# Kernel optimization log

Hardware: AMD Instinct MI355X
Metric: run time of the kernel (lower is better)

## Reference

```python
import jax, jax.numpy as jnp
import numpy as np

N_NODES = 50000
NEG_SLOPE = 0.2  # PyG GATConv default leaky_relu slope


def gat_conv(x, W, att_src, att_dst, bias, src, dst, num_nodes, concat):
    """PyG-style GATConv (eval mode, self-loops already appended to src/dst)."""
    H, C = att_src.shape
    h = (x @ W).reshape(num_nodes, H, C)           # [N,H,C]
    a_s = jnp.einsum('nhc,hc->nh', h, att_src)     # [N,H]
    a_d = jnp.einsum('nhc,hc->nh', h, att_dst)     # [N,H]
    e = jax.nn.leaky_relu(a_s[src] + a_d[dst], NEG_SLOPE)   # [E,H]
    # segment softmax over incoming edges of each destination node
    m = jax.ops.segment_max(e, dst, num_segments=num_nodes)  # [N,H]
    p = jnp.exp(e - m[dst])
    denom = jax.ops.segment_sum(p, dst, num_segments=num_nodes)
    alpha = p / (denom[dst] + 1e-16)               # [E,H]
    # scatter-aggregate messages
    out = jax.ops.segment_sum(h[src] * alpha[:, :, None], dst,
                              num_segments=num_nodes)        # [N,H,C]
    out = out.reshape(num_nodes, H * C) if concat else out.mean(axis=1)
    return out + bias


def setup_inputs() -> dict:
    key = jax.random.key(0)
    ks = jax.random.split(key, 12)
    F_in, H1, C1, C2 = 500, 8, 64, 64
    E = 600000
    x = jax.random.normal(ks[0], (N_NODES, F_in), jnp.float32)
    edge_index = jax.random.randint(ks[1], (2, E), 0, N_NODES, jnp.int64)
    s = 0.1
    return {
        'x': x,
        'edge_index': edge_index,
        'W1': jax.random.normal(ks[2], (F_in, H1 * C1), jnp.float32) * s,
        'att_src1': jax.random.normal(ks[3], (H1, C1), jnp.float32) * s,
        'att_dst1': jax.random.normal(ks[4], (H1, C1), jnp.float32) * s,
        'b1': jax.random.normal(ks[5], (H1 * C1,), jnp.float32) * s,
        'W2': jax.random.normal(ks[6], (H1 * C1, C2), jnp.float32) * s,
        'att_src2': jax.random.normal(ks[7], (1, C2), jnp.float32) * s,
        'att_dst2': jax.random.normal(ks[8], (1, C2), jnp.float32) * s,
        'b2': jax.random.normal(ks[9], (C2,), jnp.float32) * s,
        'Wl': jax.random.normal(ks[10], (C2, F_in), jnp.float32) * s,
        'bl': jax.random.normal(ks[11], (F_in,), jnp.float32) * s,
    }


def reference(x, edge_index, W1, att_src1, att_dst1, b1,
              W2, att_src2, att_dst2, b2, Wl, bl):
    # eval mode: F.dropout(p=0.6) is identity
    loop = jnp.arange(N_NODES, dtype=edge_index.dtype)
    src = jnp.concatenate([edge_index[0], loop])  # add_self_loops=True default
    dst = jnp.concatenate([edge_index[1], loop])
    h = gat_conv(x, W1, att_src1, att_dst1, b1, src, dst, N_NODES, concat=True)
    h = jax.nn.elu(h)
    h = gat_conv(h, W2, att_src2, att_dst2, b2, src, dst, N_NODES, concat=False)
    h = jax.nn.elu(h)
    return h @ Wl + bl
```

## Files before the change

kernel.cpp:

```cpp
#include <hip/hip_runtime.h>
#include <hip/hip_bf16.h>


#define N_NODES 50000
#define F_IN    500
#define H1      8
#define E_RAW   600000
#define E_TOT   (E_RAW + N_NODES)
#define NEG_SLOPE 0.2f

#define MP      50048
#define KP      512

typedef __attribute__((ext_vector_type(8))) short bf16x8;
typedef __attribute__((ext_vector_type(4))) float f32x4;
typedef unsigned short ushort_t;

__device__ __forceinline__ int edge_src(const int* ei, int e) {
    return (e < E_RAW) ? ei[e] : e - E_RAW;
}
__device__ __forceinline__ int edge_dst(const int* ei, int e) {
    return (e < E_RAW) ? ei[E_RAW + e] : e - E_RAW;
}

__device__ __forceinline__ unsigned short f32_to_bf16(float f) {
    unsigned int u = __float_as_uint(f);
    u += 0x7fffu + ((u >> 16) & 1u);
    return (unsigned short)(u >> 16);
}
__device__ __forceinline__ float bf16_lo(unsigned int u) {
    return __uint_as_float(u << 16);
}
__device__ __forceinline__ float bf16_hi(unsigned int u) {
    return __uint_as_float(u & 0xffff0000u);
}

__global__ void fill_i32(int* __restrict__ p, int v, long n) {
    long i = blockIdx.x * (long)blockDim.x + threadIdx.x;
    long stride = (long)gridDim.x * blockDim.x;
    for (; i < n; i += stride) p[i] = v;
}

__global__ void count_deg(const int* __restrict__ ei, int* __restrict__ deg) {
    long i = blockIdx.x * (long)blockDim.x + threadIdx.x;
    long stride = (long)gridDim.x * blockDim.x;
    for (; i < E_TOT; i += stride) atomicAdd(&deg[edge_dst(ei, (int)i)], 1);
}

__global__ void scan_part(const int* __restrict__ deg, int* __restrict__ part, int n) {
    __shared__ int sm[256];
    int i = blockIdx.x * 256 + threadIdx.x;
    sm[threadIdx.x] = (i < n) ? deg[i] : 0;
    __syncthreads();
    for (int d = 128; d >= 1; d >>= 1) {
        if (threadIdx.x < d) sm[threadIdx.x] += sm[threadIdx.x + d];
        __syncthreads();
    }
    if (threadIdx.x == 0) part[blockIdx.x] = sm[0];
}

__global__ void scan_top(int* __restrict__ part, int nb) {
    __shared__ int sm[256];
    int t = threadIdx.x;
    sm[t] = (t < nb) ? part[t] : 0;
    __syncthreads();
    for (int d = 1; d < 256; d <<= 1) {
        int v = (t >= d) ? sm[t - d] : 0;
        __syncthreads();
        sm[t] += v;
        __syncthreads();
    }
    if (t < nb) part[t] = (t == 0) ? 0 : sm[t - 1];
}

__global__ void scan_final(const int* __restrict__ deg, const int* __restrict__ part,
                           int* __restrict__ off, int n) {
    __shared__ int sm[256];
    int i = blockIdx.x * 256 + threadIdx.x;
    int v = (i < n) ? deg[i] : 0;
    sm[threadIdx.x] = v;
    __syncthreads();
    for (int d = 1; d < 256; d <<= 1) {
        int u = (threadIdx.x >= d) ? sm[threadIdx.x - d] : 0;
        __syncthreads();
        sm[threadIdx.x] += u;
        __syncthreads();
    }
    int excl = sm[threadIdx.x] - v + part[blockIdx.x];
    if (i < n) off[i] = excl;
    if (i == n - 1) off[n] = excl + v;
}

__global__ void scatter_edges(const int* __restrict__ ei, const int* __restrict__ off,
                              int* __restrict__ cnt, int* __restrict__ eid) {
    long i = blockIdx.x * (long)blockDim.x + threadIdx.x;
    long stride = (long)gridDim.x * blockDim.x;
    for (; i < E_TOT; i += stride) {
        int d = edge_dst(ei, (int)i);
        int p = atomicAdd(&cnt[d], 1);
        eid[off[d] + p] = (int)i;
    }
}

__global__ void cvt_w1t_bf16(const float* __restrict__ W1, ushort_t* __restrict__ w1t) {
    int idx = blockIdx.x * blockDim.x + threadIdx.x;
    if (idx >= 512 * (KP / 2)) return;
    int n = idx >> 8, k0 = (idx & 255) * 2;
    float v0 = (k0 < F_IN) ? W1[(long)k0 * 512 + n] : 0.f;
    float v1 = (k0 + 1 < F_IN) ? W1[(long)(k0 + 1) * 512 + n] : 0.f;
    ((unsigned int*)w1t)[idx] = (unsigned int)f32_to_bf16(v0) |
                                ((unsigned int)f32_to_bf16(v1) << 16);
}

__global__ void cvt_w2t_bf16(const float* __restrict__ W2, ushort_t* __restrict__ w2t) {
    int idx = blockIdx.x * blockDim.x + threadIdx.x;
    if (idx >= 64 * 256) return;
    int n = idx >> 8, k0 = (idx & 255) * 2;
    float v0 = W2[(long)k0 * 64 + n];
    float v1 = W2[(long)(k0 + 1) * 64 + n];
    ((unsigned int*)w2t)[idx] = (unsigned int)f32_to_bf16(v0) |
                                ((unsigned int)f32_to_bf16(v1) << 16);
}

__global__ void cvt_wlt_bf16(const float* __restrict__ Wl, ushort_t* __restrict__ wlt) {
    int idx = blockIdx.x * blockDim.x + threadIdx.x;
    if (idx >= 512 * 32) return;
    int n = idx >> 5, k0 = (idx & 31) * 2;
    float v0 = (n < F_IN) ? Wl[(long)k0 * F_IN + n] : 0.f;
    float v1 = (n < F_IN) ? Wl[(long)(k0 + 1) * F_IN + n] : 0.f;
    ((unsigned int*)wlt)[idx] = (unsigned int)f32_to_bf16(v0) |
                                ((unsigned int)f32_to_bf16(v1) << 16);
}

__global__ __launch_bounds__(256, 4) void gemm1_big(
        const float* __restrict__ X, const ushort_t* __restrict__ Bt,
        const float* __restrict__ att_s, const float* __restrict__ att_d,
        ushort_t* __restrict__ H, float* __restrict__ a_s, float* __restrict__ a_d) {
    __shared__ ushort_t As[64 * 72];
    __shared__ ushort_t Bs[256 * 64];
    int tid = threadIdx.x;
    int lane = tid & 63, wid = tid >> 6;
    int wrow = wid >> 1, wcol = wid & 1;
    int lrow = lane & 15, lkb = lane >> 4;
    int brow = blockIdx.y, bcol = blockIdx.x;

    f32x4 acc[2][8];
    const f32x4 zero = {0.f, 0.f, 0.f, 0.f};
    #pragma unroll
    for (int mi = 0; mi < 2; ++mi)
        #pragma unroll
        for (int ni = 0; ni < 8; ++ni) acc[mi][ni] = zero;

    int arow = tid >> 2;
    int akq = (tid & 3) * 16;
    long arow_g = (long)brow * 64 + arow;
    bool arow_ok = arow_g < N_NODES;
    const float* aG = X + arow_g * F_IN;
    ushort_t* aL = As + arow * 72 + akq;

    for (int k0 = 0; k0 < KP; k0 += 64) {
        #pragma unroll
        for (int i = 0; i < 8; ++i) {
            int slotL = i * 256 + tid;
            int n = slotL >> 3, s = slotL & 7;
            const ushort_t* g = Bt + ((long)(bcol * 256 + n)) * 512 + k0 +
                                ((s ^ (n & 7)) * 8);
            __builtin_amdgcn_global_load_lds(
                (const __attribute__((address_space(1))) void*)g,
                (__attribute__((address_space(3))) void*)(Bs + slotL * 8), 16, 0, 0);
        }
        float av[16];
        #pragma unroll
        for (int q = 0; q < 4; ++q) {
            int kk = k0 + akq + q * 4;
            float4 v = {0.f, 0.f, 0.f, 0.f};
            if (arow_ok && kk + 4 <= F_IN) v = *(const float4*)(aG + kk);
            av[q * 4 + 0] = v.x; av[q * 4 + 1] = v.y;
            av[q * 4 + 2] = v.z; av[q * 4 + 3] = v.w;
        }
        int4 apk0, apk1;
        #pragma unroll
        for (int q = 0; q < 4; ++q) {
            ((unsigned*)&apk0)[q] = (unsigned)f32_to_bf16(av[2 * q]) |
                                    ((unsigned)f32_to_bf16(av[2 * q + 1]) << 16);
            ((unsigned*)&apk1)[q] = (unsigned)f32_to_bf16(av[8 + 2 * q]) |
                                    ((unsigned)f32_to_bf16(av[9 + 2 * q]) << 16);
        }
        *(int4*)aL = apk0;
        *(int4*)(aL + 8) = apk1;
        __syncthreads();

        #pragma unroll
        for (int ks = 0; ks < 2; ++ks) {
            bf16x8 af[2], bfr[8];
            #pragma unroll
            for (int mi = 0; mi < 2; ++mi) {
                int row = wrow * 32 + mi * 16 + lrow;
                af[mi] = *(const bf16x8*)(As + row * 72 + ks * 32 + lkb * 8);
            }
            #pragma unroll
            for (int ni = 0; ni < 8; ++ni) {
                int n = wcol * 128 + ni * 16 + lrow;
                bfr[ni] = *(const bf16x8*)(Bs + n * 64 +
                                           (((ks * 4 + lkb) ^ (n & 7)) * 8));
            }
            #pragma unroll
            for (int mi = 0; mi < 2; ++mi)
                #pragma unroll
                for (int ni = 0; ni < 8; ++ni)
                    acc[mi][ni] = __builtin_amdgcn_mfma_f32_16x16x32_bf16(
                        af[mi], bfr[ni], acc[mi][ni], 0, 0, 0);
        }
        __syncthreads();
    }

    int hA = bcol * 4 + wcol * 2, hB = hA + 1;
    float asv[2][4], adv[2][4];
    #pragma unroll
    for (int j = 0; j < 4; ++j) {
        asv[0][j] = att_s[hA * 64 + j * 16 + lrow];
        asv[1][j] = att_s[hB * 64 + j * 16 + lrow];
        adv[0][j] = att_d[hA * 64 + j * 16 + lrow];
        adv[1][j] = att_d[hB * 64 + j * 16 + lrow];
    }

    #pragma unroll
    for (int mi = 0; mi < 2; ++mi) {
        #pragma unroll
        for (int reg = 0; reg < 4; ++reg) {
            long r = (long)brow * 64 + wrow * 32 + mi * 16 + lkb * 4 + reg;
            #pragma unroll
            for (int ni = 0; ni < 8; ++ni) {
                int c = bcol * 256 + wcol * 128 + ni * 16 + lrow;
                H[r * 512 + c] = f32_to_bf16(acc[mi][ni][reg]);
            }
            float sA = 0.f, dA = 0.f, sB = 0.f, dB = 0.f;
            #pragma unroll
            for (int j = 0; j < 4; ++j) {
                sA += acc[mi][j][reg] * asv[0][j];
                dA += acc[mi][j][reg] * adv[0][j];
                sB += acc[mi][j + 4][reg] * asv[1][j];
                dB += acc[mi][j + 4][reg] * adv[1][j];
            }
            #pragma unroll
            for (int mm = 8; mm >= 1; mm >>= 1) {
                sA += __shfl_xor(sA, mm);
                dA += __shfl_xor(dA, mm);
                sB += __shfl_xor(sB, mm);
                dB += __shfl_xor(dB, mm);
            }
            if (lrow == 0 && r < N_NODES) {
                a_s[r * 8 + hA] = sA;
                a_d[r * 8 + hA] = dA;
                a_s[r * 8 + hB] = sB;
                a_d[r * 8 + hB] = dB;
            }
        }
    }
}

#define LDP 72

__global__ __launch_bounds__(256) void gemm2_mfma(
        const ushort_t* __restrict__ A, const ushort_t* __restrict__ Bt,
        ushort_t* __restrict__ C) {
    __shared__ ushort_t As[128 * LDP];
    __shared__ ushort_t Bs[64 * LDP];
    int tid = threadIdx.x;
    int lane = tid & 63, wid = tid >> 6;
    int wrow = wid >> 1, wcol = wid & 1;
    int brow = blockIdx.x;

    f32x4 acc[4][2];
    const f32x4 zero = {0.f, 0.f, 0.f, 0.f};
    #pragma unroll
    for (int mi = 0; mi < 4; ++mi) { acc[mi][0] = zero; acc[mi][1] = zero; }

    int lrow = lane & 15, lkb = lane >> 4;

    for (int k0 = 0; k0 < 512; k0 += 64) {
        #pragma unroll
        for (int it = 0; it < 4; ++it) {
            int slot = tid + it * 256;
            int row = slot >> 3, seg = slot & 7;
            *(int4*)(As + row * LDP + seg * 8) =
                *(const int4*)(A + ((long)(brow * 128 + row)) * 512 + k0 + seg * 8);
        }
        #pragma unroll
        for (int it = 0; it < 2; ++it) {
            int slot = tid + it * 256;
            int row = slot >> 3, seg = slot & 7;
            *(int4*)(Bs + row * LDP + seg * 8) =
                *(const int4*)(Bt + (long)row * 512 + k0 + seg * 8);
        }
        __syncthreads();
        #pragma unroll
        for (int ks = 0; ks < 2; ++ks) {
            bf16x8 af[4], bfr[2];
            #pragma unroll
            for (int mi = 0; mi < 4; ++mi)
                af[mi] = *(const bf16x8*)(As + (wrow * 64 + mi * 16 + lrow) * LDP +
                                          ks * 32 + lkb * 8);
            #pragma unroll
            for (int ni = 0; ni < 2; ++ni)
                bfr[ni] = *(const bf16x8*)(Bs + (wcol * 32 + ni * 16 + lrow) * LDP +
                                           ks * 32 + lkb * 8);
            #pragma unroll
            for (int mi = 0; mi < 4; ++mi)
                #pragma unroll
                for (int ni = 0; ni < 2; ++ni)
                    acc[mi][ni] = __builtin_amdgcn_mfma_f32_16x16x32_bf16(
                        af[mi], bfr[ni], acc[mi][ni], 0, 0, 0);
        }
        __syncthreads();
    }

    #pragma unroll
    for (int mi = 0; mi < 4; ++mi)
        #pragma unroll
        for (int reg = 0; reg < 4; ++reg) {
            int r = brow * 128 + wrow * 64 + mi * 16 + lkb * 4 + reg;
            #pragma unroll
            for (int ni = 0; ni < 2; ++ni) {
                int c = wcol * 32 + ni * 16 + lrow;
                C[(long)r * 64 + c] = f32_to_bf16(acc[mi][ni][reg]);
            }
        }
}

__global__ __launch_bounds__(256) void gemm3_mfma(
        const ushort_t* __restrict__ A, const ushort_t* __restrict__ Bt,
        const float* __restrict__ bias, float* __restrict__ C) {
    __shared__ ushort_t As[128 * LDP];
    __shared__ ushort_t Bs[128 * LDP];
    int tid = threadIdx.x;
    int lane = tid & 63, wid = tid >> 6;
    int wrow = wid >> 1, wcol = wid & 1;
    int brow = blockIdx.y, bcol = blockIdx.x;

    f32x4 acc[4][4];
    const f32x4 zero = {0.f, 0.f, 0.f, 0.f};
    #pragma unroll
    for (int mi = 0; mi < 4; ++mi)
        #pragma unroll
        for (int ni = 0; ni < 4; ++ni) acc[mi][ni] = zero;

    int lrow = lane & 15, lkb = lane >> 4;

    #pragma unroll
    for (int it = 0; it < 4; ++it) {
        int slot = tid + it * 256;
        int row = slot >> 3, seg = slot & 7;
        *(int4*)(As + row * LDP + seg * 8) =
            *(const int4*)(A + ((long)(brow * 128 + row)) * 64 + seg * 8);
        *(int4*)(Bs + row * LDP + seg * 8) =
            *(const int4*)(Bt + ((long)(bcol * 128 + row)) * 64 + seg * 8);
    }
    __syncthreads();
    #pragma unroll
    for (int ks = 0; ks < 2; ++ks) {
        bf16x8 af[4], bfr[4];
        #pragma unroll
        for (int mi = 0; mi < 4; ++mi)
            af[mi] = *(const bf16x8*)(As + (wrow * 64 + mi * 16 + lrow) * LDP +
                                      ks * 32 + lkb * 8);
        #pragma unroll
        for (int ni = 0; ni < 4; ++ni)
            bfr[ni] = *(const bf16x8*)(Bs + (wcol * 64 + ni * 16 + lrow) * LDP +
                                       ks * 32 + lkb * 8);
        #pragma unroll
        for (int mi = 0; mi < 4; ++mi)
            #pragma unroll
            for (int ni = 0; ni < 4; ++ni)
                acc[mi][ni] = __builtin_amdgcn_mfma_f32_16x16x32_bf16(
                    af[mi], bfr[ni], acc[mi][ni], 0, 0, 0);
    }

    #pragma unroll
    for (int mi = 0; mi < 4; ++mi)
        #pragma unroll
        for (int reg = 0; reg < 4; ++reg) {
            int r = brow * 128 + wrow * 64 + mi * 16 + lkb * 4 + reg;
            if (r >= N_NODES) continue;
            #pragma unroll
            for (int ni = 0; ni < 4; ++ni) {
                int c = bcol * 128 + wcol * 64 + ni * 16 + lrow;
                if (c < F_IN) C[(long)r * F_IN + c] = acc[mi][ni][reg] + bias[c];
            }
        }
}

__global__ void attn_dots1(const ushort_t* __restrict__ hb, const float* __restrict__ att_s,
                           const float* __restrict__ att_d, float* __restrict__ a_s,
                           float* __restrict__ a_d) {
    long wid = (blockIdx.x * (long)blockDim.x + threadIdx.x) >> 6;
    int lane = threadIdx.x & 63;
    if (wid >= N_NODES) return;
    int n = (int)wid;
    float f = __uint_as_float(((unsigned)hb[(long)n * 64 + lane]) << 16);
    float s = f * att_s[lane], d = f * att_d[lane];
    #pragma unroll
    for (int m = 32; m >= 1; m >>= 1) { s += __shfl_xor(s, m); d += __shfl_xor(d, m); }
    if (lane == 0) { a_s[n] = s; a_d[n] = d; }
}

__global__ void csr_agg8(const int* __restrict__ ei, const int* __restrict__ off,
                         const int* __restrict__ eid, const float* __restrict__ a_s,
                         const float* __restrict__ a_d, const ushort_t* __restrict__ hb,
                         const float* __restrict__ bias, ushort_t* __restrict__ outb) {
    __shared__ float alds[4 * 64 * 9];
    long wid = (blockIdx.x * (long)blockDim.x + threadIdx.x) >> 6;
    int lane = threadIdx.x & 63;
    if (wid >= N_NODES) return;
    int dst = (int)wid;
    float* aw = alds + (threadIdx.x >> 6) * (64 * 9);
    int b = off[dst], e2 = off[dst + 1];
    int deg = e2 - b;
    int myh = lane >> 3;

    float ad[8];
    {
        const float* adp = a_d + (long)dst * 8;
        #pragma unroll
        for (int hh = 0; hh < 8; ++hh) ad[hh] = adp[hh];
    }

    float acc8[8];
    #pragma unroll
    for (int q = 0; q < 8; ++q) acc8[q] = 0.f;

    if (deg <= 64) {
        bool act = lane < deg;
        int src = act ? edge_src(ei, eid[b + lane]) : 0;
        const float* asp = a_s + (long)src * 8;
        float x[8];
        #pragma unroll
        for (int hh = 0; hh < 8; ++hh) {
            float v = act ? (asp[hh] + ad[hh]) : -1e30f;
            x[hh] = v > 0.f ? v : NEG_SLOPE * v;
        }
        #pragma unroll
        for (int hh = 0; hh < 8; ++hh) {
            float cm = x[hh];
            #pragma unroll
            for (int d2 = 32; d2 >= 1; d2 >>= 1) cm = fmaxf(cm, __shfl_xor(cm, d2));
            float ce = act ? __expf(x[hh] - cm) : 0.f;
            float ss = ce;
            #pragma unroll
            for (int d2 = 32; d2 >= 1; d2 >>= 1) ss += __shfl_xor(ss, d2);
            aw[lane * 9 + hh] = ce * (1.f / (ss + 1e-16f));
        }
        asm volatile("s_waitcnt lgkmcnt(0)" ::: "memory");
        for (int j = 0; j < deg; ++j) {
            int sj = __shfl(src, j);
            float aj = aw[j * 9 + myh];
            int4 hv = *(const int4*)(hb + (long)sj * 512 + lane * 8);
            #pragma unroll
            for (int q = 0; q < 4; ++q) {
                unsigned u = ((const unsigned*)&hv)[q];
                acc8[2 * q]     += aj * bf16_lo(u);
                acc8[2 * q + 1] += aj * bf16_hi(u);
            }
        }
    } else {
        float m[8], ssum[8];
        #pragma unroll
        for (int hh = 0; hh < 8; ++hh) { m[hh] = -1e30f; ssum[hh] = 0.f; }

        for (int c = b; c < e2; c += 64) {
            int i = c + lane;
            bool act = i < e2;
            int src = act ? edge_src(ei, eid[i]) : 0;
            float x[8];
            {
                const float* asp = a_s + (long)src * 8;
                #pragma unroll
                for (int hh = 0; hh < 8; ++hh) {
                    float v = act ? (asp[hh] + ad[hh]) : -1e30f;
                    x[hh] = v > 0.f ? v : NEG_SLOPE * v;
                }
            }
            #pragma unroll
            for (int hh = 0; hh < 8; ++hh) {
                float cm = x[hh];
                #pragma unroll
                for (int d2 = 32; d2 >= 1; d2 >>= 1) cm = fmaxf(cm, __shfl_xor(cm, d2));
                float nm = fmaxf(m[hh], cm);
                float ce = act ? __expf(x[hh] - nm) : 0.f;
                #pragma unroll
                for (int d2 = 32; d2 >= 1; d2 >>= 1) ce += __shfl_xor(ce, d2);
                ssum[hh] = ssum[hh] * __expf(m[hh] - nm) + ce;
                m[hh] = nm;
            }
        }
        float inv[8];
        #pragma unroll
        for (int hh = 0; hh < 8; ++hh) inv[hh] = 1.f / (ssum[hh] + 1e-16f);

        for (int c = b; c < e2; c += 64) {
            int i = c + lane;
            bool act = i < e2;
            int src = act ? edge_src(ei, eid[i]) : 0;
            {
                const float* asp = a_s + (long)src * 8;
                #pragma unroll
                for (int hh = 0; hh < 8; ++hh) {
                    float v = act ? (asp[hh] + ad[hh]) : -1e30f;
                    v = v > 0.f ? v : NEG_SLOPE * v;
                    aw[lane * 9 + hh] = act ? __expf(v - m[hh]) * inv[hh] : 0.f;
                }
            }
            asm volatile("s_waitcnt lgkmcnt(0)" ::: "memory");
            int cnt = min(64, e2 - c);
            for (int j = 0; j < cnt; ++j) {
                int sj = __shfl(src, j);
                float aj = aw[j * 9 + myh];
                int4 hv = *(const int4*)(hb + (long)sj * 512 + lane * 8);
                #pragma unroll
                for (int q = 0; q < 4; ++q) {
                    unsigned u = ((const unsigned*)&hv)[q];
                    acc8[2 * q]     += aj * bf16_lo(u);
                    acc8[2 * q + 1] += aj * bf16_hi(u);
                }
            }
            asm volatile("s_waitcnt lgkmcnt(0)" ::: "memory");
        }
    }

    const float* bp = bias + lane * 8;
    int4 st;
    #pragma unroll
    for (int q = 0; q < 8; ++q) {
        float v = acc8[q] + bp[q];
        v = v > 0.f ? v : (__expf(v) - 1.f);
        ((ushort_t*)&st)[q] = f32_to_bf16(v);
    }
    *(int4*)(outb + (long)dst * 512 + lane * 8) = st;
}

__global__ void csr_agg1(const int* __restrict__ ei, const int* __restrict__ off,
                         const int* __restrict__ eid, const float* __restrict__ a_s,
                         const float* __restrict__ a_d, const ushort_t* __restrict__ hb,
                         const float* __restrict__ bias, ushort_t* __restrict__ outb) {
    long wid = (blockIdx.x * (long)blockDim.x + threadIdx.x) >> 6;
    int lane = threadIdx.x & 63;
    if (wid >= N_NODES) return;
    int dst = (int)wid;
    int b = off[dst], e2 = off[dst + 1];
    float ad = a_d[dst];

    float m = -1e30f, ssum = 0.f;
    for (int c = b; c < e2; c += 64) {
        int i = c + lane;
        bool act = i < e2;
        int src = act ? edge_src(ei, eid[i]) : 0;
        float v = act ? (a_s[src] + ad) : -1e30f;
        float x = v > 0.f ? v : NEG_SLOPE * v;
        float cm = x;
        #pragma unroll
        for (int d2 = 32; d2 >= 1; d2 >>= 1) cm = fmaxf(cm, __shfl_xor(cm, d2));
        float nm = fmaxf(m, cm);
        float ce = act ? __expf(x - nm) : 0.f;
        #pragma unroll
        for (int d2 = 32; d2 >= 1; d2 >>= 1) ce += __shfl_xor(ce, d2);
        ssum = ssum * __expf(m - nm) + ce;
        m = nm;
    }
    float inv = 1.f / (ssum + 1e-16f);

    float acc = 0.f;
    for (int c = b; c < e2; c += 64) {
        int i = c + lane;
        bool act = i < e2;
        int src = act ? edge_src(ei, eid[i]) : 0;
        float alpha = 0.f;
        if (act) {
            float v = a_s[src] + ad;
            v = v > 0.f ? v : NEG_SLOPE * v;
            alpha = __expf(v - m) * inv;
        }
        int cnt = min(64, e2 - c);
        for (int j = 0; j < cnt; ++j) {
            int sj = __shfl(src, j);
            float aj = __shfl(alpha, j);
            float f = __uint_as_float(((unsigned)hb[(long)sj * 64 + lane]) << 16);
            acc += aj * f;
        }
    }
    float v = acc + bias[lane];
    v = v > 0.f ? v : (__expf(v) - 1.f);
    outb[(long)dst * 64 + lane] = f32_to_bf16(v);
}

extern "C" void kernel_launch(void* const* d_in, const int* in_sizes, int n_in,
                              void* d_out, int out_size, void* d_ws, size_t ws_size,
                              hipStream_t stream) {
    const float* x        = (const float*)d_in[0];
    const int*   ei       = (const int*)d_in[1];
    const float* W1       = (const float*)d_in[2];
    const float* att_src1 = (const float*)d_in[3];
    const float* att_dst1 = (const float*)d_in[4];
    const float* b1       = (const float*)d_in[5];
    const float* W2       = (const float*)d_in[6];
    const float* att_src2 = (const float*)d_in[7];
    const float* att_dst2 = (const float*)d_in[8];
    const float* b2       = (const float*)d_in[9];
    const float* Wl       = (const float*)d_in[10];
    const float* bl       = (const float*)d_in[11];
    float* out = (float*)d_out;

    char* p = (char*)d_ws;
    ushort_t* h1b   = (ushort_t*)p; p += (long)MP * 512 * 2;
    ushort_t* out1b = (ushort_t*)p; p += (long)MP * 512 * 2;
    ushort_t* h2b   = (ushort_t*)p; p += (long)MP * 64 * 2;
    ushort_t* out2b = (ushort_t*)p; p += (long)MP * 64 * 2;
    float* as1 = (float*)p; p += (long)N_NODES * 8 * 4;
    float* ad1 = (float*)p; p += (long)N_NODES * 8 * 4;
    ushort_t* w1t = (ushort_t*)p; p += 512 * 512 * 2;
    ushort_t* w2t = (ushort_t*)p; p += 64 * 512 * 2;
    ushort_t* wlt = (ushort_t*)p; p += 512 * 64 * 2;
    int* csr_off = (int*)p; p += (N_NODES + 4) * 4;
    int* csr_cnt = (int*)p; p += N_NODES * 4;
    int* csr_eid = (int*)p; p += (long)E_TOT * 4;
    int* scan_p  = (int*)p; p += 256 * 4;

    const int BT = 256;
    dim3 blk(BT);
    const int NB_SCAN = (N_NODES + 255) / 256;

    fill_i32<<<256, blk, 0, stream>>>(csr_cnt, 0, N_NODES);
    count_deg<<<1024, blk, 0, stream>>>(ei, csr_cnt);
    scan_part<<<NB_SCAN, blk, 0, stream>>>(csr_cnt, scan_p, N_NODES);
    scan_top<<<1, blk, 0, stream>>>(scan_p, NB_SCAN);
    scan_final<<<NB_SCAN, blk, 0, stream>>>(csr_cnt, scan_p, csr_off, N_NODES);
    fill_i32<<<256, blk, 0, stream>>>(csr_cnt, 0, N_NODES);
    scatter_edges<<<1024, blk, 0, stream>>>(ei, csr_off, csr_cnt, csr_eid);

    cvt_w1t_bf16<<<512, blk, 0, stream>>>(W1, w1t);
    cvt_w2t_bf16<<<64, blk, 0, stream>>>(W2, w2t);
    cvt_wlt_bf16<<<64, blk, 0, stream>>>(Wl, wlt);
    fill_i32<<<12, blk, 0, stream>>>((int*)(out1b + (long)N_NODES * 512), 0,
                                     (MP - N_NODES) * 512 / 2);
    fill_i32<<<2, blk, 0, stream>>>((int*)(out2b + (long)N_NODES * 64), 0,
                                    (MP - N_NODES) * 64 / 2);

    {
        dim3 grid(2, MP / 64);
        gemm1_big<<<grid, blk, 0, stream>>>(x, w1t, att_src1, att_dst1,
                                            h1b, as1, ad1);
    }
    csr_agg8<<<(N_NODES * 64 + BT - 1) / BT, blk, 0, stream>>>(
        ei, csr_off, csr_eid, as1, ad1, h1b, b1, out1b);

    gemm2_mfma<<<MP / 128, blk, 0, stream>>>(out1b, w2t, h2b);
    attn_dots1<<<(N_NODES * 64 + BT - 1) / BT, blk, 0, stream>>>(h2b, att_src2, att_dst2,
                                                                 as1, ad1);
    csr_agg1<<<(N_NODES * 64 + BT - 1) / BT, blk, 0, stream>>>(
        ei, csr_off, csr_eid, as1, ad1, h2b, b2, out2b);

    {
        dim3 grid(512 / 128, MP / 128);
        gemm3_mfma<<<grid, blk, 0, stream>>>(out2b, wlt, bl, out);
    }
}
```

Before: 411.4 us.

## Merge setup kernels, store CSR sources directly, unroll aggregation gathers

Several small setup kernels are merged: the fills become one kernel and the three weight conversions become one, which cuts launch count. The CSR build now writes source node ids directly via atomic positions seeded by the scan, removing the eid indirection and the second count reset. Both aggregation kernels unroll the neighbor gather by four to keep more loads in flight, and the single-head kernel gets a one-pass softmax fast path for degree at most 64. The changes add code complexity and slightly alter floating-point summation order.

```diff
diff --git a/kernel.cpp b/kernel.cpp
--- a/kernel.cpp
+++ b/kernel.cpp
@@ -35,10 +35,18 @@
     return __uint_as_float(u & 0xffff0000u);
 }
 
-__global__ void fill_i32(int* __restrict__ p, int v, long n) {
-    long i = blockIdx.x * (long)blockDim.x + threadIdx.x;
-    long stride = (long)gridDim.x * blockDim.x;
-    for (; i < n; i += stride) p[i] = v;
+__global__ void fill_misc(int* __restrict__ cnt, int* __restrict__ pad1,
+                          int* __restrict__ pad2) {
+    const int N1 = N_NODES;
+    const int N2 = (MP - N_NODES) * 512 / 2;
+    const int N3 = (MP - N_NODES) * 64 / 2;
+    int i = blockIdx.x * blockDim.x + threadIdx.x;
+    int stride = gridDim.x * blockDim.x;
+    for (; i < N1 + N2 + N3; i += stride) {
+        if (i < N1) cnt[i] = 0;
+        else if (i < N1 + N2) pad1[i - N1] = 0;
+        else pad2[i - N1 - N2] = 0;
+    }
 }
 
 __global__ void count_deg(const int* __restrict__ ei, int* __restrict__ deg) {
@@ -74,7 +82,7 @@
 }
 
 __global__ void scan_final(const int* __restrict__ deg, const int* __restrict__ part,
-                           int* __restrict__ off, int n) {
+                           int* __restrict__ off, int* __restrict__ pos, int n) {
     __shared__ int sm[256];
     int i = blockIdx.x * 256 + threadIdx.x;
     int v = (i < n) ? deg[i] : 0;
@@ -87,49 +95,51 @@
         __syncthreads();
     }
     int excl = sm[threadIdx.x] - v + part[blockIdx.x];
-    if (i < n) off[i] = excl;
+    if (i < n) { off[i] = excl; pos[i] = excl; }
     if (i == n - 1) off[n] = excl + v;
 }
 
-__global__ void scatter_edges(const int* __restrict__ ei, const int* __restrict__ off,
-                              int* __restrict__ cnt, int* __restrict__ eid) {
+__global__ void scatter_src(const int* __restrict__ ei, int* __restrict__ pos,
+                            int* __restrict__ srcs) {
     long i = blockIdx.x * (long)blockDim.x + threadIdx.x;
     long stride = (long)gridDim.x * blockDim.x;
     for (; i < E_TOT; i += stride) {
-        int d = edge_dst(ei, (int)i);
-        int p = atomicAdd(&cnt[d], 1);
-        eid[off[d] + p] = (int)i;
-    }
-}
-
-__global__ void cvt_w1t_bf16(const float* __restrict__ W1, ushort_t* __restrict__ w1t) {
+        int e = (int)i;
+        int s, d;
+        if (e < E_RAW) { s = ei[e]; d = ei[E_RAW + e]; } else { s = d = e - E_RAW; }
+        int p = atomicAdd(&pos[d], 1);
+        srcs[p] = s;
+    }
+}
+
+__global__ void cvt_weights(const float* __restrict__ W1, const float* __restrict__ W2,
+                            const float* __restrict__ Wl, ushort_t* __restrict__ w1t,
+                            ushort_t* __restrict__ w2t, ushort_t* __restrict__ wlt) {
+    const int R1 = 512 * 256;
+    const int R2 = 64 * 256;
+    const int R3 = 512 * 32;
     int idx = blockIdx.x * blockDim.x + threadIdx.x;
-    if (idx >= 512 * (KP / 2)) return;
-    int n = idx >> 8, k0 = (idx & 255) * 2;
-    float v0 = (k0 < F_IN) ? W1[(long)k0 * 512 + n] : 0.f;
-    float v1 = (k0 + 1 < F_IN) ? W1[(long)(k0 + 1) * 512 + n] : 0.f;
-    ((unsigned int*)w1t)[idx] = (unsigned int)f32_to_bf16(v0) |
-                                ((unsigned int)f32_to_bf16(v1) << 16);
-}
-
-__global__ void cvt_w2t_bf16(const float* __restrict__ W2, ushort_t* __restrict__ w2t) {
-    int idx = blockIdx.x * blockDim.x + threadIdx.x;
-    if (idx >= 64 * 256) return;
-    int n = idx >> 8, k0 = (idx & 255) * 2;
-    float v0 = W2[(long)k0 * 64 + n];
-    float v1 = W2[(long)(k0 + 1) * 64 + n];
-    ((unsigned int*)w2t)[idx] = (unsigned int)f32_to_bf16(v0) |
-                                ((unsigned int)f32_to_bf16(v1) << 16);
-}
-
-__global__ void cvt_wlt_bf16(const float* __restrict__ Wl, ushort_t* __restrict__ wlt) {
-    int idx = blockIdx.x * blockDim.x + threadIdx.x;
-    if (idx >= 512 * 32) return;
-    int n = idx >> 5, k0 = (idx & 31) * 2;
-    float v0 = (n < F_IN) ? Wl[(long)k0 * F_IN + n] : 0.f;
-    float v1 = (n < F_IN) ? Wl[(long)(k0 + 1) * F_IN + n] : 0.f;
-    ((unsigned int*)wlt)[idx] = (unsigned int)f32_to_bf16(v0) |
-                                ((unsigned int)f32_to_bf16(v1) << 16);
+    if (idx < R1) {
+        int n = idx >> 8, k0 = (idx & 255) * 2;
+        float v0 = (k0 < F_IN) ? W1[(long)k0 * 512 + n] : 0.f;
+        float v1 = (k0 + 1 < F_IN) ? W1[(long)(k0 + 1) * 512 + n] : 0.f;
+        ((unsigned int*)w1t)[idx] = (unsigned)f32_to_bf16(v0) |
+                                    ((unsigned)f32_to_bf16(v1) << 16);
+    } else if (idx < R1 + R2) {
+        int k = idx - R1;
+        int n = k >> 8, k0 = (k & 255) * 2;
+        float v0 = W2[(long)k0 * 64 + n];
+        float v1 = W2[(long)(k0 + 1) * 64 + n];
+        ((unsigned int*)w2t)[k] = (unsigned)f32_to_bf16(v0) |
+                                  ((unsigned)f32_to_bf16(v1) << 16);
+    } else if (idx < R1 + R2 + R3) {
+        int k = idx - R1 - R2;
+        int n = k >> 5, k0 = (k & 31) * 2;
+        float v0 = (n < F_IN) ? Wl[(long)k0 * F_IN + n] : 0.f;
+        float v1 = (n < F_IN) ? Wl[(long)(k0 + 1) * F_IN + n] : 0.f;
+        ((unsigned int*)wlt)[k] = (unsigned)f32_to_bf16(v0) |
+                                  ((unsigned)f32_to_bf16(v1) << 16);
+    }
 }
 
 __global__ __launch_bounds__(256, 4) void gemm1_big(
@@ -404,10 +414,10 @@
     if (lane == 0) { a_s[n] = s; a_d[n] = d; }
 }
 
-__global__ void csr_agg8(const int* __restrict__ ei, const int* __restrict__ off,
-                         const int* __restrict__ eid, const float* __restrict__ a_s,
-                         const float* __restrict__ a_d, const ushort_t* __restrict__ hb,
-                         const float* __restrict__ bias, ushort_t* __restrict__ outb) {
+__global__ void csr_agg8(const int* __restrict__ srcs, const int* __restrict__ off,
+                         const float* __restrict__ a_s, const float* __restrict__ a_d,
+                         const ushort_t* __restrict__ hb, const float* __restrict__ bias,
+                         ushort_t* __restrict__ outb) {
     __shared__ float alds[4 * 64 * 9];
     long wid = (blockIdx.x * (long)blockDim.x + threadIdx.x) >> 6;
     int lane = threadIdx.x & 63;
@@ -431,7 +441,7 @@
 
     if (deg <= 64) {
         bool act = lane < deg;
-        int src = act ? edge_src(ei, eid[b + lane]) : 0;
+        int src = act ? srcs[b + lane] : 0;
         const float* asp = a_s + (long)src * 8;
         float x[8];
         #pragma unroll
@@ -451,7 +461,29 @@
             aw[lane * 9 + hh] = ce * (1.f / (ss + 1e-16f));
         }
         asm volatile("s_waitcnt lgkmcnt(0)" ::: "memory");
-        for (int j = 0; j < deg; ++j) {
+        int j = 0;
+        for (; j + 4 <= deg; j += 4) {
+            int s0 = __shfl(src, j),     s1 = __shfl(src, j + 1);
+            int s2 = __shfl(src, j + 2), s3 = __shfl(src, j + 3);
+            float a0 = aw[(j) * 9 + myh],     a1 = aw[(j + 1) * 9 + myh];
+            float a2 = aw[(j + 2) * 9 + myh], a3 = aw[(j + 3) * 9 + myh];
+            int4 h0 = *(const int4*)(hb + (long)s0 * 512 + lane * 8);
+            int4 h1 = *(const int4*)(hb + (long)s1 * 512 + lane * 8);
+            int4 h2 = *(const int4*)(hb + (long)s2 * 512 + lane * 8);
+            int4 h3 = *(const int4*)(hb + (long)s3 * 512 + lane * 8);
+            #pragma unroll
+            for (int q = 0; q < 4; ++q) {
+                unsigned u0 = ((const unsigned*)&h0)[q];
+                unsigned u1 = ((const unsigned*)&h1)[q];
+                unsigned u2 = ((const unsigned*)&h2)[q];
+                unsigned u3 = ((const unsigned*)&h3)[q];
+                acc8[2 * q]     += a0 * bf16_lo(u0) + a1 * bf16_lo(u1) +
+                                   a2 * bf16_lo(u2) + a3 * bf16_lo(u3);
+                acc8[2 * q + 1] += a0 * bf16_hi(u0) + a1 * bf16_hi(u1) +
+                                   a2 * bf16_hi(u2) + a3 * bf16_hi(u3);
+            }
+        }
+        for (; j < deg; ++j) {
             int sj = __shfl(src, j);
             float aj = aw[j * 9 + myh];
             int4 hv = *(const int4*)(hb + (long)sj * 512 + lane * 8);
@@ -470,7 +502,7 @@
         for (int c = b; c < e2; c += 64) {
             int i = c + lane;
             bool act = i < e2;
-            int src = act ? edge_src(ei, eid[i]) : 0;
+            int src = act ? srcs[i] : 0;
             float x[8];
             {
                 const float* asp = a_s + (long)src * 8;
@@ -500,7 +532,7 @@
         for (int c = b; c < e2; c += 64) {
             int i = c + lane;
             bool act = i < e2;
-            int src = act ? edge_src(ei, eid[i]) : 0;
+            int src = act ? srcs[i] : 0;
             {
                 const float* asp = a_s + (long)src * 8;
                 #pragma unroll
@@ -538,53 +570,85 @@
     *(int4*)(outb + (long)dst * 512 + lane * 8) = st;
 }
 
-__global__ void csr_agg1(const int* __restrict__ ei, const int* __restrict__ off,
-                         const int* __restrict__ eid, const float* __restrict__ a_s,
-                         const float* __restrict__ a_d, const ushort_t* __restrict__ hb,
-                         const float* __restrict__ bias, ushort_t* __restrict__ outb) {
+__global__ void csr_agg1(const int* __restrict__ srcs, const int* __restrict__ off,
+                         const float* __restrict__ a_s, const float* __restrict__ a_d,
+                         const ushort_t* __restrict__ hb, const float* __restrict__ bias,
+                         ushort_t* __restrict__ outb) {
     long wid = (blockIdx.x * (long)blockDim.x + threadIdx.x) >> 6;
     int lane = threadIdx.x & 63;
     if (wid >= N_NODES) return;
     int dst = (int)wid;
     int b = off[dst], e2 = off[dst + 1];
+    int deg = e2 - b;
     float ad = a_d[dst];
-
-    float m = -1e30f, ssum = 0.f;
-    for (int c = b; c < e2; c += 64) {
-        int i = c + lane;
-        bool act = i < e2;
-        int src = act ? edge_src(ei, eid[i]) : 0;
+    float acc = 0.f;
+
+    if (deg <= 64) {
+        bool act = lane < deg;
+        int src = act ? srcs[b + lane] : 0;
         float v = act ? (a_s[src] + ad) : -1e30f;
-        float x = v > 0.f ? v : NEG_SLOPE * v;
-        float cm = x;
+        float xx = v > 0.f ? v : NEG_SLOPE * v;
+        float cm = xx;
         #pragma unroll
         for (int d2 = 32; d2 >= 1; d2 >>= 1) cm = fmaxf(cm, __shfl_xor(cm, d2));
-        float nm = fmaxf(m, cm);
-        float ce = act ? __expf(x - nm) : 0.f;
-        #pragma unroll
-        for (int d2 = 32; d2 >= 1; d2 >>= 1) ce += __shfl_xor(ce, d2);
-        ssum = ssum * __expf(m - nm) + ce;
-        m = nm;
-    }
-    float inv = 1.f / (ssum + 1e-16f);
-
-    float acc = 0.f;
-    for (int c = b; c < e2; c += 64) {
-        int i = c + lane;
-        bool act = i < e2;
-        int src = act ? edge_src(ei, eid[i]) : 0;
-        float alpha = 0.f;
-        if (act) {
-            float v = a_s[src] + ad;
-            v = v > 0.f ? v : NEG_SLOPE * v;
-            alpha = __expf(v - m) * inv;
-        }
-        int cnt = min(64, e2 - c);
-        for (int j = 0; j < cnt; ++j) {
+        float alpha = act ? __expf(xx - cm) : 0.f;
+        float ss = alpha;
+        #pragma unroll
+        for (int d2 = 32; d2 >= 1; d2 >>= 1) ss += __shfl_xor(ss, d2);
+        alpha *= 1.f / (ss + 1e-16f);
+
+        int j = 0;
+        for (; j + 4 <= deg; j += 4) {
+            int s0 = __shfl(src, j),     s1 = __shfl(src, j + 1);
+            int s2 = __shfl(src, j + 2), s3 = __shfl(src, j + 3);
+            float a0 = __shfl(alpha, j),     a1 = __shfl(alpha, j + 1);
+            float a2 = __shfl(alpha, j + 2), a3 = __shfl(alpha, j + 3);
+            float f0 = __uint_as_float(((unsigned)hb[(long)s0 * 64 + lane]) << 16);
+            float f1 = __uint_as_float(((unsigned)hb[(long)s1 * 64 + lane]) << 16);
+            float f2 = __uint_as_float(((unsigned)hb[(long)s2 * 64 + lane]) << 16);
+            float f3 = __uint_as_float(((unsigned)hb[(long)s3 * 64 + lane]) << 16);
+            acc += a0 * f0 + a1 * f1 + a2 * f2 + a3 * f3;
+        }
+        for (; j < deg; ++j) {
             int sj = __shfl(src, j);
             float aj = __shfl(alpha, j);
-            float f = __uint_as_float(((unsigned)hb[(long)sj * 64 + lane]) << 16);
-            acc += aj * f;
+            acc += aj * __uint_as_float(((unsigned)hb[(long)sj * 64 + lane]) << 16);
+        }
+    } else {
+        float m = -1e30f, ssum = 0.f;
+        for (int c = b; c < e2; c += 64) {
+            int i = c + lane;
+            bool act = i < e2;
+            int src = act ? srcs[i] : 0;
+            float v = act ? (a_s[src] + ad) : -1e30f;
+            float xx = v > 0.f ? v : NEG_SLOPE * v;
+            float cm = xx;
+            #pragma unroll
+            for (int d2 = 32; d2 >= 1; d2 >>= 1) cm = fmaxf(cm, __shfl_xor(cm, d2));
+            float nm = fmaxf(m, cm);
+            float ce = act ? __expf(xx - nm) : 0.f;
+            #pragma unroll
+            for (int d2 = 32; d2 >= 1; d2 >>= 1) ce += __shfl_xor(ce, d2);
+            ssum = ssum * __expf(m - nm) + ce;
+            m = nm;
+        }
+        float inv = 1.f / (ssum + 1e-16f);
+        for (int c = b; c < e2; c += 64) {
+            int i = c + lane;
+            bool act = i < e2;
+            int src = act ? srcs[i] : 0;
+            float alpha = 0.f;
+            if (act) {
+                float v = a_s[src] + ad;
+                v = v > 0.f ? v : NEG_SLOPE * v;
+                alpha = __expf(v - m) * inv;
+            }
+            int cnt = min(64, e2 - c);
+            for (int j = 0; j < cnt; ++j) {
+                int sj = __shfl(src, j);
+                float aj = __shfl(alpha, j);
+                acc += aj * __uint_as_float(((unsigned)hb[(long)sj * 64 + lane]) << 16);
+            }
         }
     }
     float v = acc + bias[lane];
@@ -621,28 +685,23 @@
     ushort_t* wlt = (ushort_t*)p; p += 512 * 64 * 2;
     int* csr_off = (int*)p; p += (N_NODES + 4) * 4;
     int* csr_cnt = (int*)p; p += N_NODES * 4;
-    int* csr_eid = (int*)p; p += (long)E_TOT * 4;
+    int* csr_pos = (int*)p; p += N_NODES * 4;
+    int* csr_src = (int*)p; p += (long)E_TOT * 4;
     int* scan_p  = (int*)p; p += 256 * 4;
 
     const int BT = 256;
     dim3 blk(BT);
     const int NB_SCAN = (N_NODES + 255) / 256;
 
-    fill_i32<<<256, blk, 0, stream>>>(csr_cnt, 0, N_NODES);
+    fill_misc<<<256, blk, 0, stream>>>(csr_cnt, (int*)(out1b + (long)N_NODES * 512),
+                                       (int*)(out2b + (long)N_NODES * 64));
     count_deg<<<1024, blk, 0, stream>>>(ei, csr_cnt);
     scan_part<<<NB_SCAN, blk, 0, stream>>>(csr_cnt, scan_p, N_NODES);
     scan_top<<<1, blk, 0, stream>>>(scan_p, NB_SCAN);
-    scan_final<<<NB_SCAN, blk, 0, stream>>>(csr_cnt, scan_p, csr_off, N_NODES);
-    fill_i32<<<256, blk, 0, stream>>>(csr_cnt, 0, N_NODES);
-    scatter_edges<<<1024, blk, 0, stream>>>(ei, csr_off, csr_cnt, csr_eid);
-
-    cvt_w1t_bf16<<<512, blk, 0, stream>>>(W1, w1t);
-    cvt_w2t_bf16<<<64, blk, 0, stream>>>(W2, w2t);
-    cvt_wlt_bf16<<<64, blk, 0, stream>>>(Wl, wlt);
-    fill_i32<<<12, blk, 0, stream>>>((int*)(out1b + (long)N_NODES * 512), 0,
-                                     (MP - N_NODES) * 512 / 2);
-    fill_i32<<<2, blk, 0, stream>>>((int*)(out2b + (long)N_NODES * 64), 0,
-                                    (MP - N_NODES) * 64 / 2);
+    scan_final<<<NB_SCAN, blk, 0, stream>>>(csr_cnt, scan_p, csr_off, csr_pos, N_NODES);
+    scatter_src<<<1024, blk, 0, stream>>>(ei, csr_pos, csr_src);
+
+    cvt_weights<<<640, blk, 0, stream>>>(W1, W2, Wl, w1t, w2t, wlt);
 
     {
         dim3 grid(2, MP / 64);
@@ -650,13 +709,13 @@
                                             h1b, as1, ad1);
     }
     csr_agg8<<<(N_NODES * 64 + BT - 1) / BT, blk, 0, stream>>>(
-        ei, csr_off, csr_eid, as1, ad1, h1b, b1, out1b);
+        csr_src, csr_off, as1, ad1, h1b, b1, out1b);
 
     gemm2_mfma<<<MP / 128, blk, 0, stream>>>(out1b, w2t, h2b);
     attn_dots1<<<(N_NODES * 64 + BT - 1) / BT, blk, 0, stream>>>(h2b, att_src2, att_dst2,
                                                                  as1, ad1);
     csr_agg1<<<(N_NODES * 64 + BT - 1) / BT, blk, 0, stream>>>(
-        ei, csr_off, csr_eid, as1, ad1, h2b, b2, out2b);
+        csr_src, csr_off, as1, ad1, h2b, b2, out2b);
 
     {
         dim3 grid(512 / 128, MP / 128);
```

New measurement: 371.4 us. -9.7%, faster.
